# Kernel tuning notes

Measured on AMD Instinct MI355X. Metric: run time of the kernel, lower is better.

The kernel has to match this reference:

```python
import jax, jax.numpy as jnp
import numpy as np

B, D, N, F = 2048, 512, 100000, 64
NEG = -1000000.0


def setup_inputs() -> dict:
    key = jax.random.key(0)
    k1, k2, k3, k4 = jax.random.split(key, 4)
    q = jax.random.normal(k1, (B, D), dtype=jnp.float32)
    rhs = jax.random.normal(k2, (D, N), dtype=jnp.float32)
    queries = jax.random.randint(k3, (B, 3), 0, N, dtype=jnp.int64)
    filter_idx = jax.random.randint(k4, (B, F), 0, N, dtype=jnp.int64)
    return {"q": q, "rhs": rhs, "queries": queries, "filter_idx": filter_idx}


def reference(q, rhs, queries, filter_idx):
    # targets[i] = score of the true triple = q[i] . rhs[:, true_rhs[i]]
    true_rhs = queries[:, 2]                         # [B]
    targets = jnp.einsum('bd,bd->b', q, rhs[:, true_rhs].T)  # [B]

    scores = q @ rhs                                  # [B, N]

    # filtered ranking: mask out known true tails + the query's own tail
    rows = jnp.arange(scores.shape[0])[:, None]       # [B, 1]
    scores = scores.at[rows, filter_idx].set(NEG)
    scores = scores.at[jnp.arange(scores.shape[0]), true_rhs].set(NEG)

    # rank = 1 + number of candidates scoring >= the true triple
    ranks = 1.0 + jnp.sum((scores >= targets[:, None]).astype(jnp.float32), axis=1)
    return ranks
```

## Files before the change

kernel.cpp:

```cpp
#include <hip/hip_runtime.h>
#include <hip/hip_bf16.h>

#define B_ 2048
#define D_ 512
#define N_ 100000
#define F_ 64
#define NEGV (-1000000.0f)

typedef __bf16 bfx8 __attribute__((ext_vector_type(8)));
typedef float f32x4 __attribute__((ext_vector_type(4)));
typedef unsigned short u16x8 __attribute__((ext_vector_type(8)));

static __device__ __forceinline__ unsigned short f2bf(float f) {
  unsigned u = __float_as_uint(f);
  unsigned r = (u + 0x7fffu + ((u >> 16) & 1u)) >> 16;
  return (unsigned short)r;
}
static __device__ __forceinline__ float bf2f(unsigned short u) {
  return __uint_as_float(((unsigned)u) << 16);
}

static __device__ __forceinline__ void async_copy16(const void* g, void* l) {
  __builtin_amdgcn_global_load_lds((const __attribute__((address_space(1))) void*)g,
                                   (__attribute__((address_space(3))) void*)l, 16, 0, 0);
}

__global__ void targets_init(const float* __restrict__ q, const float* __restrict__ rhs,
                             const int* __restrict__ queries, float* __restrict__ targets,
                             float* __restrict__ out) {
  int b = blockIdx.x * 4 + (threadIdx.x >> 6);
  int lane = threadIdx.x & 63;
  int p = queries[b * 3 + 2];
  float s = 0.f;
  for (int d = lane; d < D_; d += 64) s += q[b * D_ + d] * rhs[(size_t)d * N_ + p];
  for (int off = 32; off; off >>= 1) s += __shfl_down(s, off, 64);
  if (lane == 0) { targets[b] = s; out[b] = 1.0f; }
}

__global__ void convert_q(const float* __restrict__ q, unsigned short* __restrict__ qb) {
  int i = blockIdx.x * blockDim.x + threadIdx.x;
  const float4* q4 = (const float4*)q;
  float4 v = q4[i];
  ushort4 o;
  o.x = f2bf(v.x); o.y = f2bf(v.y); o.z = f2bf(v.z); o.w = f2bf(v.w);
  ((ushort4*)qb)[i] = o;
}

__global__ void transpose_rhs(const float* __restrict__ rhs, unsigned short* __restrict__ rt) {
  __shared__ float tile[64][65];
  int n0 = blockIdx.x * 64, d0 = blockIdx.y * 64;
  int c = threadIdx.x & 63, r4 = threadIdx.x >> 6;
#pragma unroll
  for (int p = 0; p < 16; ++p) {
    int d = r4 + p * 4;
    int n = n0 + c;
    if (n < N_) tile[d][c] = rhs[(size_t)(d0 + d) * N_ + n];
  }
  __syncthreads();
#pragma unroll
  for (int p = 0; p < 16; ++p) {
    int nl = r4 + p * 4;
    int n = n0 + nl;
    if (n < N_) rt[(size_t)n * D_ + d0 + c] = f2bf(tile[c][nl]);
  }
}

__global__ void __launch_bounds__(256) gemm_count(
    const unsigned short* __restrict__ qb,
    const unsigned short* __restrict__ rt,
    const float* __restrict__ targets,
    float* __restrict__ out) {
  __shared__ unsigned short As[128 * 32];
  __shared__ unsigned short Bs[128 * 32];
  __shared__ float sT[128];
  __shared__ int cnt[128];

  int tid = threadIdx.x;
  int m0 = blockIdx.x * 128;
  int n0 = blockIdx.y * 128;

  if (tid < 128) { sT[tid] = targets[m0 + tid]; cnt[tid] = 0; }

  int w = tid >> 6, lane = tid & 63;
  int mw = (w & 1) * 64, nw = (w >> 1) * 64;
  int quad = lane >> 4, l16 = lane & 15;

  f32x4 acc[4][4];
  f32x4 z = {0.f, 0.f, 0.f, 0.f};
#pragma unroll
  for (int i = 0; i < 4; ++i)
#pragma unroll
    for (int j = 0; j < 4; ++j) acc[i][j] = z;

  for (int kt = 0; kt < 16; ++kt) {
    int k0 = kt * 32;
    __syncthreads();
#pragma unroll
    for (int i = 0; i < 2; ++i) {
      int c = i * 256 + tid;
      int m = c >> 2, k8 = (c & 3) * 8;
      const unsigned short* gp = qb + (size_t)(m0 + m) * D_ + k0 + k8;
      async_copy16(gp, As + c * 8);
    }
#pragma unroll
    for (int i = 0; i < 2; ++i) {
      int c = i * 256 + tid;
      int n = c >> 2, k8 = (c & 3) * 8;
      int ng = n0 + n; if (ng > N_ - 1) ng = N_ - 1;
      const unsigned short* gp = rt + (size_t)ng * D_ + k0 + k8;
      async_copy16(gp, Bs + c * 8);
    }
    __syncthreads();

    bfx8 a[4], b[4];
#pragma unroll
    for (int mi = 0; mi < 4; ++mi) {
      int m = mw + mi * 16 + l16;
      u16x8 au = *(const u16x8*)(As + m * 32 + quad * 8);
      a[mi] = __builtin_bit_cast(bfx8, au);
    }
#pragma unroll
    for (int ni = 0; ni < 4; ++ni) {
      int n = nw + ni * 16 + l16;
      u16x8 bu = *(const u16x8*)(Bs + n * 32 + quad * 8);
      b[ni] = __builtin_bit_cast(bfx8, bu);
    }
#pragma unroll
    for (int mi = 0; mi < 4; ++mi)
#pragma unroll
      for (int ni = 0; ni < 4; ++ni)
        acc[mi][ni] = __builtin_amdgcn_mfma_f32_16x16x32_bf16(a[mi], b[ni], acc[mi][ni], 0, 0, 0);
  }

#pragma unroll
  for (int mi = 0; mi < 4; ++mi) {
#pragma unroll
    for (int reg = 0; reg < 4; ++reg) {
      int rl = mw + mi * 16 + quad * 4 + reg;
      float t = sT[rl];
      int c = 0;
#pragma unroll
      for (int ni = 0; ni < 4; ++ni) {
        int col = n0 + nw + ni * 16 + l16;
        if (col < N_ && acc[mi][ni][reg] >= t) c++;
      }
      if (c) atomicAdd(&cnt[rl], c);
    }
  }
  __syncthreads();
  if (tid < 128 && cnt[tid]) atomicAdd(&out[m0 + tid], (float)cnt[tid]);
}

__global__ void corrections(const unsigned short* __restrict__ qb,
                            const unsigned short* __restrict__ rt,
                            const int* __restrict__ queries,
                            const int* __restrict__ filt,
                            const float* __restrict__ targets,
                            float* __restrict__ out) {
  int b = blockIdx.x;
  int tid = threadIdx.x;
  __shared__ int idx[F_ + 1];
  __shared__ float red[128];
  if (tid < F_) idx[tid] = filt[b * F_ + tid];
  if (tid == F_) idx[F_] = queries[b * 3 + 2];
  __syncthreads();
  float corr = 0.f;
  float t = targets[b];
  if (tid <= F_) {
    int p = idx[tid];
    bool uniq = true;
    for (int j = 0; j < tid; ++j)
      if (idx[j] == p) uniq = false;
    if (uniq) {
      float s = 0.f;
      const u16x8* qr = (const u16x8*)(qb + (size_t)b * D_);
      const u16x8* rr = (const u16x8*)(rt + (size_t)p * D_);
      for (int i = 0; i < D_ / 8; ++i) {
        u16x8 qv = qr[i], rv = rr[i];
#pragma unroll
        for (int j = 0; j < 8; ++j) s += bf2f(qv[j]) * bf2f(rv[j]);
      }
      corr = (NEGV >= t ? 1.f : 0.f) - (s >= t ? 1.f : 0.f);
    }
  }
  red[tid] = corr;
  __syncthreads();
  if (tid == 0) {
    float tot = 0.f;
    for (int i = 0; i < 128; ++i) tot += red[i];
    if (tot != 0.f) atomicAdd(&out[b], tot);
  }
}

__global__ void fallback_count(const float* __restrict__ q, const float* __restrict__ rhs,
                               const int* __restrict__ queries, const int* __restrict__ filt,
                               const float* __restrict__ targets, float* __restrict__ out) {
  int b = blockIdx.y;
  int n = blockIdx.x * 256 + threadIdx.x;
  __shared__ float qs[D_];
  __shared__ int idx[F_ + 1];
  __shared__ int cnt;
  for (int d = threadIdx.x; d < D_; d += 256) qs[d] = q[b * D_ + d];
  if (threadIdx.x < F_) idx[threadIdx.x] = filt[b * F_ + threadIdx.x];
  if (threadIdx.x == F_) idx[F_] = queries[b * 3 + 2];
  if (threadIdx.x == 0) cnt = 0;
  __syncthreads();
  if (n < N_) {
    float t = targets[b];
    float s = 0.f;
    for (int d = 0; d < D_; ++d) s += qs[d] * rhs[(size_t)d * N_ + n];
    bool member = false;
    for (int j = 0; j <= F_; ++j)
      if (idx[j] == n) member = true;
    float sv = member ? NEGV : s;
    if (sv >= t) atomicAdd(&cnt, 1);
  }
  __syncthreads();
  if (threadIdx.x == 0 && cnt) atomicAdd(&out[b], (float)cnt);
}

extern "C" void kernel_launch(void* const* d_in, const int* in_sizes, int n_in,
                              void* d_out, int out_size, void* d_ws, size_t ws_size,
                              hipStream_t stream) {
  const float* q = (const float*)d_in[0];
  const float* rhs = (const float*)d_in[1];
  const int* queries = (const int*)d_in[2];
  const int* filt = (const int*)d_in[3];
  float* out = (float*)d_out;

  char* wsb = (char*)d_ws;
  float* targets = (float*)wsb;
  unsigned short* qb = (unsigned short*)(wsb + 8192);
  unsigned short* rt = (unsigned short*)(wsb + 8192 + (size_t)B_ * D_ * 2);
  size_t need = 8192 + (size_t)B_ * D_ * 2 + (size_t)N_ * D_ * 2;

  targets_init<<<B_ / 4, 256, 0, stream>>>(q, rhs, queries, targets, out);

  if (ws_size >= need) {
    convert_q<<<(B_ * D_ / 4) / 256, 256, 0, stream>>>(q, qb);
    transpose_rhs<<<dim3((N_ + 63) / 64, D_ / 64), 256, 0, stream>>>(rhs, rt);
    gemm_count<<<dim3(B_ / 128, (N_ + 127) / 128), 256, 0, stream>>>(qb, rt, targets, out);
    corrections<<<B_, 128, 0, stream>>>(qb, rt, queries, filt, targets, out);
  } else {
    fallback_count<<<dim3((N_ + 255) / 256, B_), 256, 0, stream>>>(q, rhs, queries, filt, targets, out);
  }
}
```

Before: 640.0 us.

## Swizzle GEMM LDS tiles, vectorize transpose stores, widen targets and corrections parallelism

XOR-swizzles the 16-byte chunks of the A and B LDS tiles in the GEMM so fragment reads spread across banks instead of colliding. The rhs transpose now writes four bf16 values per store, and each target dot product is split across a full 256-thread block. The corrections kernel gives each filter index a whole wavefront with a shuffle reduction instead of one serial thread. These changes aim at LDS bank conflicts, narrow stores and serial latency, in exchange for extra index arithmetic and more blocks.

```diff
diff --git a/kernel.cpp b/kernel.cpp
--- a/kernel.cpp
+++ b/kernel.cpp
@@ -28,13 +28,19 @@
 __global__ void targets_init(const float* __restrict__ q, const float* __restrict__ rhs,
                              const int* __restrict__ queries, float* __restrict__ targets,
                              float* __restrict__ out) {
-  int b = blockIdx.x * 4 + (threadIdx.x >> 6);
-  int lane = threadIdx.x & 63;
+  __shared__ float wsum[4];
+  int b = blockIdx.x;
+  int tid = threadIdx.x, lane = tid & 63, w = tid >> 6;
   int p = queries[b * 3 + 2];
   float s = 0.f;
-  for (int d = lane; d < D_; d += 64) s += q[b * D_ + d] * rhs[(size_t)d * N_ + p];
+  for (int d = tid; d < D_; d += 256) s += q[b * D_ + d] * rhs[(size_t)d * N_ + p];
   for (int off = 32; off; off >>= 1) s += __shfl_down(s, off, 64);
-  if (lane == 0) { targets[b] = s; out[b] = 1.0f; }
+  if (lane == 0) wsum[w] = s;
+  __syncthreads();
+  if (tid == 0) {
+    targets[b] = wsum[0] + wsum[1] + wsum[2] + wsum[3];
+    out[b] = 1.0f;
+  }
 }
 
 __global__ void convert_q(const float* __restrict__ q, unsigned short* __restrict__ qb) {
@@ -58,10 +64,17 @@
   }
   __syncthreads();
 #pragma unroll
-  for (int p = 0; p < 16; ++p) {
-    int nl = r4 + p * 4;
-    int n = n0 + nl;
-    if (n < N_) rt[(size_t)n * D_ + d0 + c] = f2bf(tile[c][nl]);
+  for (int p = 0; p < 4; ++p) {
+    int e = p * 256 + threadIdx.x;
+    int n = e >> 4, dg = e & 15;
+    if (n0 + n < N_) {
+      ushort4 o;
+      o.x = f2bf(tile[dg * 4 + 0][n]);
+      o.y = f2bf(tile[dg * 4 + 1][n]);
+      o.z = f2bf(tile[dg * 4 + 2][n]);
+      o.w = f2bf(tile[dg * 4 + 3][n]);
+      *(ushort4*)(rt + (size_t)(n0 + n) * D_ + d0 + dg * 4) = o;
+    }
   }
 }
 
@@ -98,16 +111,18 @@
 #pragma unroll
     for (int i = 0; i < 2; ++i) {
       int c = i * 256 + tid;
-      int m = c >> 2, k8 = (c & 3) * 8;
-      const unsigned short* gp = qb + (size_t)(m0 + m) * D_ + k0 + k8;
+      int m = c >> 2, jj = c & 3;
+      int j = jj ^ (m & 3);
+      const unsigned short* gp = qb + (size_t)(m0 + m) * D_ + k0 + j * 8;
       async_copy16(gp, As + c * 8);
     }
 #pragma unroll
     for (int i = 0; i < 2; ++i) {
       int c = i * 256 + tid;
-      int n = c >> 2, k8 = (c & 3) * 8;
+      int n = c >> 2, jj = c & 3;
+      int j = jj ^ (n & 3);
       int ng = n0 + n; if (ng > N_ - 1) ng = N_ - 1;
-      const unsigned short* gp = rt + (size_t)ng * D_ + k0 + k8;
+      const unsigned short* gp = rt + (size_t)ng * D_ + k0 + j * 8;
       async_copy16(gp, Bs + c * 8);
     }
     __syncthreads();
@@ -116,13 +131,15 @@
 #pragma unroll
     for (int mi = 0; mi < 4; ++mi) {
       int m = mw + mi * 16 + l16;
-      u16x8 au = *(const u16x8*)(As + m * 32 + quad * 8);
+      int slot = m * 4 + (quad ^ (m & 3));
+      u16x8 au = *(const u16x8*)(As + slot * 8);
       a[mi] = __builtin_bit_cast(bfx8, au);
     }
 #pragma unroll
     for (int ni = 0; ni < 4; ++ni) {
       int n = nw + ni * 16 + l16;
-      u16x8 bu = *(const u16x8*)(Bs + n * 32 + quad * 8);
+      int slot = n * 4 + (quad ^ (n & 3));
+      u16x8 bu = *(const u16x8*)(Bs + slot * 8);
       b[ni] = __builtin_bit_cast(bfx8, bu);
     }
 #pragma unroll
@@ -159,37 +176,31 @@
                             float* __restrict__ out) {
   int b = blockIdx.x;
   int tid = threadIdx.x;
+  int w = tid >> 6, lane = tid & 63;
   __shared__ int idx[F_ + 1];
-  __shared__ float red[128];
   if (tid < F_) idx[tid] = filt[b * F_ + tid];
   if (tid == F_) idx[F_] = queries[b * 3 + 2];
   __syncthreads();
+  float t = targets[b];
   float corr = 0.f;
-  float t = targets[b];
-  if (tid <= F_) {
-    int p = idx[tid];
+  const u16x8* qrow = (const u16x8*)(qb + (size_t)b * D_);
+  for (int ii = w; ii <= F_; ii += 4) {
+    int p = idx[ii];
     bool uniq = true;
-    for (int j = 0; j < tid; ++j)
+    for (int j = 0; j < ii; ++j)
       if (idx[j] == p) uniq = false;
     if (uniq) {
+      u16x8 qv = qrow[lane];
+      u16x8 rv = ((const u16x8*)(rt + (size_t)p * D_))[lane];
       float s = 0.f;
-      const u16x8* qr = (const u16x8*)(qb + (size_t)b * D_);
-      const u16x8* rr = (const u16x8*)(rt + (size_t)p * D_);
-      for (int i = 0; i < D_ / 8; ++i) {
-        u16x8 qv = qr[i], rv = rr[i];
-#pragma unroll
-        for (int j = 0; j < 8; ++j) s += bf2f(qv[j]) * bf2f(rv[j]);
-      }
-      corr = (NEGV >= t ? 1.f : 0.f) - (s >= t ? 1.f : 0.f);
-    }
-  }
-  red[tid] = corr;
-  __syncthreads();
-  if (tid == 0) {
-    float tot = 0.f;
-    for (int i = 0; i < 128; ++i) tot += red[i];
-    if (tot != 0.f) atomicAdd(&out[b], tot);
-  }
+#pragma unroll
+      for (int j = 0; j < 8; ++j) s += bf2f(qv[j]) * bf2f(rv[j]);
+      for (int off = 32; off; off >>= 1) s += __shfl_down(s, off, 64);
+      if (lane == 0)
+        corr += (NEGV >= t ? 1.f : 0.f) - (s >= t ? 1.f : 0.f);
+    }
+  }
+  if (lane == 0 && corr != 0.f) atomicAdd(&out[b], corr);
 }
 
 __global__ void fallback_count(const float* __restrict__ q, const float* __restrict__ rhs,
@@ -234,13 +245,13 @@
   unsigned short* rt = (unsigned short*)(wsb + 8192 + (size_t)B_ * D_ * 2);
   size_t need = 8192 + (size_t)B_ * D_ * 2 + (size_t)N_ * D_ * 2;
 
-  targets_init<<<B_ / 4, 256, 0, stream>>>(q, rhs, queries, targets, out);
+  targets_init<<<B_, 256, 0, stream>>>(q, rhs, queries, targets, out);
 
   if (ws_size >= need) {
     convert_q<<<(B_ * D_ / 4) / 256, 256, 0, stream>>>(q, qb);
     transpose_rhs<<<dim3((N_ + 63) / 64, D_ / 64), 256, 0, stream>>>(rhs, rt);
     gemm_count<<<dim3(B_ / 128, (N_ + 127) / 128), 256, 0, stream>>>(qb, rt, targets, out);
-    corrections<<<B_, 128, 0, stream>>>(qb, rt, queries, filt, targets, out);
+    corrections<<<B_, 256, 0, stream>>>(qb, rt, queries, filt, targets, out);
   } else {
     fallback_count<<<dim3((N_ + 255) / 256, B_), 256, 0, stream>>>(q, rhs, queries, filt, targets, out);
   }
```

Result: slower. 663.3 us (+3.6%).
